# Optimization experiments

Measured on AMD Instinct MI355X. Metric: run time of the kernel, lower is better.

The kernel has to match this reference:

```python
import jax, jax.numpy as jnp
import numpy as np
from jax import lax

EPS = 1e-3  # Keras BatchNormalization default epsilon


def _hard_sigmoid(x):
    # Keras recurrent_activation default for ConvLSTM2D
    return jnp.clip(0.2 * x + 0.5, 0.0, 1.0)


def _conv(x, w, padding):
    # x: [B, Cin, H, W], w: [Cout, Cin, kh, kw]
    return lax.conv_general_dilated(
        x, w, window_strides=(1, 1), padding=padding,
        dimension_numbers=("NCHW", "OIHW", "NCHW"))


def _sympad(x):
    # tf.pad(..., [[0,0],[0,0],[0,0],[1,1],[1,1]], 'SYMMETRIC') on [B,T,C,H,W]
    return jnp.pad(x, ((0, 0), (0, 0), (0, 0), (1, 1), (1, 1)), mode="symmetric")


def _convlstm(xpad, h0, c0, W, U, b):
    # xpad: [B, T, Cin, H+2, W+2]; input conv 'VALID' -> HxW; recurrent conv 'SAME'.
    # Keras gate order along the 4F channel axis: i, f, c(g), o.
    # activation='sigmoid' (candidate/output), recurrent_activation=hard_sigmoid.
    def step(carry, x_t):
        h, c = carry
        z = _conv(x_t, W, "VALID") + _conv(h, U, "SAME") + b[None, :, None, None]
        i, f, g, o = jnp.split(z, 4, axis=1)
        c_new = _hard_sigmoid(f) * c + _hard_sigmoid(i) * jax.nn.sigmoid(g)
        h_new = _hard_sigmoid(o) * jax.nn.sigmoid(c_new)
        return (h_new, c_new), h_new

    (hT, cT), hs = lax.scan(step, (h0, c0), jnp.moveaxis(xpad, 1, 0))
    return jnp.moveaxis(hs, 0, 1), hT, cT  # [B,T,F,H,W], [B,F,H,W] x2


def setup_inputs() -> dict:
    key = jax.random.key(0)
    ks = jax.random.split(key, 5)
    B, T, C, H, Wd, F = 4, 12, 4, 60, 80, 64
    z = lambda: jnp.zeros((B, F, H, Wd), jnp.float32)
    return {
        "inputs": jax.random.normal(ks[0], (B, T, C, H, Wd), jnp.float32),
        "h1_0": z(), "c1_0": z(), "h2_0": z(), "c2_0": z(),
        "W1": jax.random.normal(ks[1], (4 * F, C, 3, 3), jnp.float32) * 0.05,
        "U1": jax.random.normal(ks[2], (4 * F, F, 3, 3), jnp.float32) * 0.05,
        "b1": jnp.zeros((4 * F,), jnp.float32),
        "W2": jax.random.normal(ks[3], (4 * F, F, 3, 3), jnp.float32) * 0.05,
        "U2": jax.random.normal(ks[4], (4 * F, F, 3, 3), jnp.float32) * 0.05,
        "b2": jnp.zeros((4 * F,), jnp.float32),
        "gamma": jnp.ones((Wd,), jnp.float32),
        "beta": jnp.zeros((Wd,), jnp.float32),
    }


def reference(inputs, h1_0, c1_0, h2_0, c2_0, W1, U1, b1, W2, U2, b2, gamma, beta):
    x, h1, c1 = _convlstm(_sympad(inputs), h1_0, c1_0, W1, U1, b1)
    # BatchNorm, Keras default axis=-1 (the W axis here), training-mode batch stats.
    mean = jnp.mean(x, axis=(0, 1, 2, 3), keepdims=True)
    var = jnp.var(x, axis=(0, 1, 2, 3), keepdims=True)
    x = (x - mean) * lax.rsqrt(var + EPS) * gamma + beta
    x, h2, c2 = _convlstm(_sympad(x), h2_0, c2_0, W2, U2, b2)
    # dropout treated as identity (deterministic reference)
    return (x, h1, c1, h2, c2)
```

## Files before the change

kernel.cpp:

```cpp
#include <hip/hip_runtime.h>
#include <hip/hip_bf16.h>

typedef __hip_bfloat16 bf16;
typedef __attribute__((ext_vector_type(8))) short sh8;
typedef __attribute__((ext_vector_type(4))) short sh4;
typedef __attribute__((ext_vector_type(4))) float f32x4;

#define HWp 4800
#define Wd 80
#define Hd 60
#define Fh 64
#define Bn 4
#define Tn 12
#define KYS 5248
#define sHT ((long)Fh*HWp)

__device__ __forceinline__ float b2f(bf16 v){ return __bfloat162float(v); }
__device__ __forceinline__ bf16 f2b(float v){ return __float2bfloat16(v); }
__device__ __forceinline__ float bits2f(short s){
    return __uint_as_float(((unsigned)(unsigned short)s) << 16);
}
__device__ __forceinline__ short f2bits(float f){
    bf16 t = f2b(f); short s; __builtin_memcpy(&s, &t, 2); return s;
}

__global__ void perm_w_kernel(const float* __restrict__ src, float* __restrict__ dst, int cin){
    int idx = blockIdx.x*256 + threadIdx.x;
    int n = 256*cin*9;
    if (idx >= n) return;
    int co = idx/(cin*9); int r = idx - co*(cin*9);
    int g = co >> 6, fo = co & 63;
    dst[(fo*4+g)*cin*9 + r] = src[idx];
}
__global__ void perm_bias_kernel(const float* __restrict__ src, float* __restrict__ dst){
    int idx = threadIdx.x;
    int g = idx >> 6, fo = idx & 63;
    dst[fo*4+g] = src[idx];
}
__global__ void pack_w_kernel(const float* __restrict__ U, short* __restrict__ Apk){
    int d = blockIdx.x*256 + threadIdx.x;
    if (d >= 147456) return;
    int j = d & 7, l = (d>>3) & 63, ct = (d>>9) & 15, oc = d >> 13;
    int o = oc >> 1, cc = oc & 1;
    int co = ct*16 + (l & 15);
    int ci = cc*32 + (l>>4)*8 + j;
    Apk[d] = f2bits(U[(co*Fh + ci)*9 + o]);
}

__global__ void copy_f32_kernel(const float* __restrict__ src, float* __restrict__ dst, int n){
    int idx = blockIdx.x*256+threadIdx.x;
    if (idx < n) dst[idx] = src[idx];
}
__global__ void copy_h_f32_kernel(const float* __restrict__ src, long bstride, float* __restrict__ dst){
    long idx = (long)blockIdx.x*256+threadIdx.x;
    long n = (long)Bn*Fh*HWp;
    if (idx >= n) return;
    long b = idx/(Fh*HWp); long r = idx - b*(Fh*HWp);
    dst[idx] = src[b*bstride + r];
}
__global__ void h0cl_kernel(const float* __restrict__ src, bf16* __restrict__ dst){
    long idx = (long)blockIdx.x*256 + threadIdx.x;
    if (idx >= (long)Bn*Fh*HWp) return;
    int fo = (int)(idx & 63);
    long rest = idx >> 6;
    int p = (int)(rest % HWp);
    int b = (int)(rest / HWp);
    dst[idx] = f2b(src[((long)b*Fh + fo)*HWp + p]);
}

__global__ void zx1_kernel(const float* __restrict__ xin,
                           const float* __restrict__ Wf,
                           const float* __restrict__ bias,
                           short* __restrict__ zx)
{
    int p = blockIdx.x*blockDim.x + threadIdx.x;
    if (p >= HWp) return;
    int fo = blockIdx.y, bt = blockIdx.z;
    int y = p / Wd, x = p - y*Wd;
    const float* wf = Wf + fo*4*4*9;
    float acc[4] = {bias[fo*4+0], bias[fo*4+1], bias[fo*4+2], bias[fo*4+3]};
    int ym = (y > 0 ? y-1 : 0)*Wd, y0 = y*Wd, yp = (y < Hd-1 ? y+1 : Hd-1)*Wd;
    int xm = (x > 0 ? x-1 : 0),    xp = (x < Wd-1 ? x+1 : Wd-1);
    for (int ci = 0; ci < 4; ++ci){
        const float* ic = xin + ((long)bt*4 + ci)*HWp;
        float v[9];
        v[0]=ic[ym+xm]; v[1]=ic[ym+x]; v[2]=ic[ym+xp];
        v[3]=ic[y0+xm]; v[4]=ic[y0+x]; v[5]=ic[y0+xp];
        v[6]=ic[yp+xm]; v[7]=ic[yp+x]; v[8]=ic[yp+xp];
        #pragma unroll
        for (int g = 0; g < 4; ++g){
            const float* w = wf + (g*4+ci)*9;
            acc[g] += v[0]*w[0]+v[1]*w[1]+v[2]*w[2]
                    + v[3]*w[3]+v[4]*w[4]+v[5]*w[5]
                    + v[6]*w[6]+v[7]*w[7]+v[8]*w[8];
        }
    }
    sh4 o4 = { f2bits(acc[0]), f2bits(acc[1]), f2bits(acc[2]), f2bits(acc[3]) };
    *(sh4*)(zx + ((long)bt*HWp + p)*256 + fo*4) = o4;
}

template<bool CLAMP>
__device__ __forceinline__ void stage_cl(const short* __restrict__ src, int y, short* lt){
    const int tid = threadIdx.x;
    #pragma unroll
    for (int it = 0; it < 8; ++it){
        int n = it*256 + tid;
        if (n < 1968){
            int row = n/656, rem = n - row*656;
            int rg = y + row - 1;
            bool rvalid = CLAMP ? true : (rg >= 0 && rg < Hd);
            rg = min(max(rg,0), Hd-1);
            int xg, cc, xl; bool cvalid = true;
            if (rem < 640){ xg = rem>>3; cc = rem&7; xl = xg+1; }
            else if (rem < 648){ xg = 0; cc = rem-640; xl = 0; cvalid = CLAMP; }
            else { xg = Wd-1; cc = rem-648; xl = 81; cvalid = CLAMP; }
            sh8 v = {0,0,0,0,0,0,0,0};
            if (rvalid && cvalid) v = *(const sh8*)(src + ((long)(rg*Wd + xg)*64 + cc*8));
            *(sh8*)(lt + row*KYS + xl*64 + ((cc ^ (xl&7))<<3)) = v;
        }
    }
}

__device__ __forceinline__ void gemm_core(const short* __restrict__ Apk, const short* lt,
                                          int wv, int lane, f32x4 acc[4][5]){
    const int lane15 = lane & 15, grp = lane >> 4;
    #pragma unroll
    for (int o = 0; o < 9; ++o){
        int ky = o/3, kx = o - 3*(o/3);
        const short* lk = lt + ky*KYS;
        #pragma unroll
        for (int c = 0; c < 2; ++c){
            sh8 bfr[5];
            #pragma unroll
            for (int pt = 0; pt < 5; ++pt){
                int xl = pt*16 + lane15 + kx;
                int cc = (c*4 + grp) ^ (xl & 7);
                bfr[pt] = *(const sh8*)(lk + xl*64 + cc*8);
            }
            const short* ab = Apk + ((long)((o*2 + c)*16 + wv))*512 + lane*8;
            #pragma unroll
            for (int g = 0; g < 4; ++g){
                sh8 af = *(const sh8*)(ab + (long)g*4*512);
                #pragma unroll
                for (int pt = 0; pt < 5; ++pt)
                    acc[g][pt] = __builtin_amdgcn_mfma_f32_16x16x32_bf16(af, bfr[pt], acc[g][pt], 0, 0, 0);
            }
        }
    }
}

template<bool WRITE_FX>
__global__ __launch_bounds__(256) void rec_step(
    const bf16* __restrict__ hprev, long h_bstride,
    const short* __restrict__ Upk,
    const short* __restrict__ zx_t, long z_bstride,
    float* __restrict__ c,
    bf16* __restrict__ hout,
    float* __restrict__ fx, long f_bstride)
{
    __shared__ short lt[3*KYS];
    int y = blockIdx.x, b = blockIdx.y;
    int tid = threadIdx.x, lane = tid & 63, wv = tid >> 6;
    int lane15 = lane & 15, grp = lane >> 4;

    stage_cl<false>((const short*)hprev + (long)b*h_bstride, y, lt);

    sh4 zq[5][4]; float cold[5][4];
    const short* zb = zx_t + (long)b*z_bstride;
    #pragma unroll
    for (int pt = 0; pt < 5; ++pt){
        int p = y*Wd + pt*16 + lane15;
        #pragma unroll
        for (int r = 0; r < 4; ++r){
            int fo = wv*16 + grp*4 + r;
            zq[pt][r] = *(const sh4*)(zb + (long)p*256 + fo*4);
            cold[pt][r] = c[((long)b*Fh + fo)*HWp + p];
        }
    }
    __syncthreads();

    f32x4 acc[4][5];
    #pragma unroll
    for (int g = 0; g < 4; ++g)
        #pragma unroll
        for (int pt = 0; pt < 5; ++pt) acc[g][pt] = (f32x4){0.f,0.f,0.f,0.f};
    gemm_core(Upk, lt, wv, lane, acc);

    #pragma unroll
    for (int pt = 0; pt < 5; ++pt){
        int p = y*Wd + pt*16 + lane15;
        #pragma unroll
        for (int r = 0; r < 4; ++r){
            int fo = wv*16 + grp*4 + r;
            float zi = acc[0][pt][r] + bits2f(zq[pt][r][0]);
            float zf = acc[1][pt][r] + bits2f(zq[pt][r][1]);
            float zg = acc[2][pt][r] + bits2f(zq[pt][r][2]);
            float zo = acc[3][pt][r] + bits2f(zq[pt][r][3]);
            float gi = fminf(fmaxf(0.2f*zi+0.5f, 0.f), 1.f);
            float gf = fminf(fmaxf(0.2f*zf+0.5f, 0.f), 1.f);
            float go = fminf(fmaxf(0.2f*zo+0.5f, 0.f), 1.f);
            float sg = 1.f/(1.f+__expf(-zg));
            float cn = gf*cold[pt][r] + gi*sg;
            float hn = go * (1.f/(1.f+__expf(-cn)));
            c[((long)b*Fh + fo)*HWp + p] = cn;
            hout[((long)b*sHT) + (long)p*64 + fo] = f2b(hn);
            if (WRITE_FX)
                fx[(long)b*f_bstride + (long)fo*HWp + p] = hn;
        }
    }
}

__global__ __launch_bounds__(256,2) void zx_mfma(
    const bf16* __restrict__ x1,
    const short* __restrict__ Wpk,
    const float* __restrict__ bias,
    short* __restrict__ zxb)
{
    __shared__ short lt[3*KYS];
    int y = blockIdx.x, img = blockIdx.y;
    int t = img / Bn, b = img - t*Bn;
    int tid = threadIdx.x, lane = tid & 63, wv = tid >> 6;
    int lane15 = lane & 15, grp = lane >> 4;
    stage_cl<true>((const short*)x1 + (long)img*sHT, y, lt);
    __syncthreads();
    f32x4 acc[4][5];
    #pragma unroll
    for (int g = 0; g < 4; ++g)
        #pragma unroll
        for (int pt = 0; pt < 5; ++pt) acc[g][pt] = (f32x4){0.f,0.f,0.f,0.f};
    gemm_core(Wpk, lt, wv, lane, acc);
    short* zb = zxb + ((long)(b*Tn + t))*HWp*256;
    #pragma unroll
    for (int pt = 0; pt < 5; ++pt){
        int p = y*Wd + pt*16 + lane15;
        #pragma unroll
        for (int r = 0; r < 4; ++r){
            int fo = wv*16 + grp*4 + r;
            sh4 o4 = { f2bits(acc[0][pt][r] + bias[fo]),
                       f2bits(acc[1][pt][r] + bias[64+fo]),
                       f2bits(acc[2][pt][r] + bias[128+fo]),
                       f2bits(acc[3][pt][r] + bias[192+fo]) };
            *(sh4*)(zb + (long)p*256 + fo*4) = o4;
        }
    }
}

#define BN_GRID 480
__global__ void bn_sum_cl(const short* __restrict__ x, float* __restrict__ sums){
    __shared__ float ls[160];
    int tid = threadIdx.x;
    if (tid < 160) ls[tid] = 0.f;
    __syncthreads();
    long gid = (long)blockIdx.x*256 + tid;
    const long nchunk = (long)Bn*Tn*HWp*8;
    float s = 0.f, q = 0.f;
    for (long ch = gid; ch < nchunk; ch += (long)BN_GRID*256){
        sh8 v = *(const sh8*)(x + ch*8);
        #pragma unroll
        for (int j = 0; j < 8; ++j){ float f = bits2f(v[j]); s += f; q += f*f; }
    }
    int w = (int)((gid>>3) % Wd);
    atomicAdd(&ls[w], s); atomicAdd(&ls[80+w], q);
    __syncthreads();
    if (tid < 160) atomicAdd(&sums[tid], ls[tid]);
}
__global__ void bn_coef_kernel(const float* __restrict__ sums, const float* __restrict__ g,
                               const float* __restrict__ bt, float* __restrict__ coef){
    int w = threadIdx.x;
    const float N = (float)(Bn*Tn*Fh*Hd);
    float mean = sums[w]/N;
    float var  = sums[80+w]/N - mean*mean;
    float sc = rsqrtf(var + 1e-3f)*g[w];
    coef[w] = sc;
    coef[80+w] = bt[w] - mean*sc;
}
__global__ void bn_apply_cl(short* __restrict__ x, const float* __restrict__ coef){
    long gid = (long)blockIdx.x*256 + threadIdx.x;
    const long nchunk = (long)Bn*Tn*HWp*8;
    int w = (int)((gid>>3) % Wd);
    float sc = coef[w], sh = coef[80+w];
    for (long ch = gid; ch < nchunk; ch += (long)BN_GRID*256){
        sh8 v = *(sh8*)(x + ch*8);
        #pragma unroll
        for (int j = 0; j < 8; ++j) v[j] = f2bits(bits2f(v[j])*sc + sh);
        *(sh8*)(x + ch*8) = v;
    }
}

extern "C" void kernel_launch(void* const* d_in, const int* in_sizes, int n_in,
                              void* d_out, int out_size, void* d_ws, size_t ws_size,
                              hipStream_t stream){
    const float* xin  = (const float*)d_in[0];
    const float* h1_0 = (const float*)d_in[1];
    const float* c1_0 = (const float*)d_in[2];
    const float* h2_0 = (const float*)d_in[3];
    const float* c2_0 = (const float*)d_in[4];
    const float* W1   = (const float*)d_in[5];
    const float* U1   = (const float*)d_in[6];
    const float* b1   = (const float*)d_in[7];
    const float* W2   = (const float*)d_in[8];
    const float* U2   = (const float*)d_in[9];
    const float* b2   = (const float*)d_in[10];
    const float* gamma= (const float*)d_in[11];
    const float* beta = (const float*)d_in[12];
    float* out = (float*)d_out;

    char* ws = (char*)d_ws;
    float* W1f = (float*)ws; ws += (size_t)256*4*9*4;
    float* b1f = (float*)ws; ws += 1024;
    short* U1p = (short*)ws; ws += (size_t)147456*2;
    short* W2p = (short*)ws; ws += (size_t)147456*2;
    short* U2p = (short*)ws; ws += (size_t)147456*2;
    float* sums= (float*)ws; ws += 1024;
    float* coef= (float*)ws; ws += 1024;
    float* cbuf= (float*)ws; ws += (size_t)Bn*Fh*HWp*4;
    bf16*  h0b = (bf16*)ws; ws += (size_t)Bn*Fh*HWp*2;
    bf16*  hdb = (bf16*)ws; ws += (size_t)2*Bn*Fh*HWp*2;
    bf16*  x1  = (bf16*)ws; ws += (size_t)Bn*Tn*Fh*HWp*2;
    short* zx  = (short*)ws; ws += (size_t)Bn*Tn*256*HWp*2;

    const long nImg = (long)Bn*Fh*HWp;
    const long xOff = (long)Bn*Tn*Fh*HWp;
    int nImgB = (int)((nImg+255)/256);

    perm_w_kernel<<<(256*4*9+255)/256, 256, 0, stream>>>(W1, W1f, 4);
    perm_bias_kernel<<<1,256,0,stream>>>(b1, b1f);
    pack_w_kernel<<<576,256,0,stream>>>(U1, U1p);
    pack_w_kernel<<<576,256,0,stream>>>(W2, W2p);
    pack_w_kernel<<<576,256,0,stream>>>(U2, U2p);

    dim3 rgrid(Hd, Bn);
    const long zstep = (long)HWp*256;
    const long zbstr = (long)Tn*HWp*256;

    dim3 zgrid1((HWp+255)/256, 64, Bn*Tn);
    zx1_kernel<<<zgrid1,256,0,stream>>>(xin, W1f, b1f, zx);
    copy_f32_kernel<<<nImgB,256,0,stream>>>(c1_0, cbuf, (int)nImg);
    h0cl_kernel<<<nImgB,256,0,stream>>>(h1_0, h0b);
    for (int t = 0; t < Tn; ++t){
        const bf16* hp = (t==0) ? h0b : x1 + (long)(t-1)*Bn*sHT;
        bf16* ho = x1 + (long)t*Bn*sHT;
        if (t == Tn-1)
            rec_step<true><<<rgrid,256,0,stream>>>(hp, sHT, U1p,
                zx + (long)t*zstep, zbstr, cbuf, ho, out + xOff, sHT);
        else
            rec_step<false><<<rgrid,256,0,stream>>>(hp, sHT, U1p,
                zx + (long)t*zstep, zbstr, cbuf, ho, nullptr, 0);
    }
    copy_f32_kernel<<<nImgB,256,0,stream>>>(cbuf, out + xOff + nImg, (int)nImg);

    hipMemsetAsync(sums, 0, 640, stream);
    bn_sum_cl<<<BN_GRID,256,0,stream>>>((const short*)x1, sums);
    bn_coef_kernel<<<1,80,0,stream>>>(sums, gamma, beta, coef);
    bn_apply_cl<<<BN_GRID,256,0,stream>>>((short*)x1, coef);

    dim3 zgrid2(Hd, Bn*Tn);
    zx_mfma<<<zgrid2,256,0,stream>>>(x1, W2p, b2, zx);
    copy_f32_kernel<<<nImgB,256,0,stream>>>(c2_0, cbuf, (int)nImg);
    h0cl_kernel<<<nImgB,256,0,stream>>>(h2_0, h0b);
    for (int t = 0; t < Tn; ++t){
        const bf16* hp = (t==0) ? h0b : hdb + (long)((t-1)&1)*Bn*sHT;
        bf16* ho = hdb + (long)(t&1)*Bn*sHT;
        rec_step<true><<<rgrid,256,0,stream>>>(hp, sHT, U2p,
            zx + (long)t*zstep, zbstr, cbuf, ho, out + (long)t*sHT, (long)Tn*sHT);
    }
    copy_h_f32_kernel<<<nImgB,256,0,stream>>>(out + (long)(Tn-1)*sHT, (long)Tn*sHT, out + xOff + 2*nImg);
    copy_f32_kernel<<<nImgB,256,0,stream>>>(cbuf, out + xOff + 3*nImg, (int)nImg);
}
```

Before: 998.4 us.

## Split recurrent step over feature halves and change zx layout to channel-major

The recurrent step kernel now launches twice as many blocks of 128 threads, each handling half of the 64 output feature tiles, so the 240-block grid becomes 480 blocks for better CU occupancy on the serial time loop. The zx gate buffer is stored feature-major (fo, pixel, gate) instead of pixel-major, making the per-lane loads contiguous across pixels. h outputs are staged through shared memory for coalesced channel-last writes. The cost is staging the 3-row halo of h twice (once per half) and an extra barrier.

New measurement: 1.004 ms. About the same (+0.6%).

```diff
diff --git a/kernel.cpp b/kernel.cpp
--- a/kernel.cpp
+++ b/kernel.cpp
@@ -14,6 +14,7 @@
 #define Tn 12
 #define KYS 5248
 #define sHT ((long)Fh*HWp)
+#define ZT  ((long)Fh*HWp*4)
 
 __device__ __forceinline__ float b2f(bf16 v){ return __bfloat162float(v); }
 __device__ __forceinline__ bf16 f2b(float v){ return __float2bfloat16(v); }
@@ -96,28 +97,24 @@
         }
     }
     sh4 o4 = { f2bits(acc[0]), f2bits(acc[1]), f2bits(acc[2]), f2bits(acc[3]) };
-    *(sh4*)(zx + ((long)bt*HWp + p)*256 + fo*4) = o4;
-}
-
-template<bool CLAMP>
+    *(sh4*)(zx + (((long)bt*Fh + fo)*HWp + p)*4) = o4;
+}
+
+template<bool CLAMP, int NT>
 __device__ __forceinline__ void stage_cl(const short* __restrict__ src, int y, short* lt){
     const int tid = threadIdx.x;
-    #pragma unroll
-    for (int it = 0; it < 8; ++it){
-        int n = it*256 + tid;
-        if (n < 1968){
-            int row = n/656, rem = n - row*656;
-            int rg = y + row - 1;
-            bool rvalid = CLAMP ? true : (rg >= 0 && rg < Hd);
-            rg = min(max(rg,0), Hd-1);
-            int xg, cc, xl; bool cvalid = true;
-            if (rem < 640){ xg = rem>>3; cc = rem&7; xl = xg+1; }
-            else if (rem < 648){ xg = 0; cc = rem-640; xl = 0; cvalid = CLAMP; }
-            else { xg = Wd-1; cc = rem-648; xl = 81; cvalid = CLAMP; }
-            sh8 v = {0,0,0,0,0,0,0,0};
-            if (rvalid && cvalid) v = *(const sh8*)(src + ((long)(rg*Wd + xg)*64 + cc*8));
-            *(sh8*)(lt + row*KYS + xl*64 + ((cc ^ (xl&7))<<3)) = v;
-        }
+    for (int n = tid; n < 1968; n += NT){
+        int row = n/656, rem = n - row*656;
+        int rg = y + row - 1;
+        bool rvalid = CLAMP ? true : (rg >= 0 && rg < Hd);
+        rg = min(max(rg,0), Hd-1);
+        int xg, cc, xl; bool cvalid = true;
+        if (rem < 640){ xg = rem>>3; cc = rem&7; xl = xg+1; }
+        else if (rem < 648){ xg = 0; cc = rem-640; xl = 0; cvalid = CLAMP; }
+        else { xg = Wd-1; cc = rem-648; xl = 81; cvalid = CLAMP; }
+        sh8 v = {0,0,0,0,0,0,0,0};
+        if (rvalid && cvalid) v = *(const sh8*)(src + ((long)(rg*Wd + xg)*64 + cc*8));
+        *(sh8*)(lt + row*KYS + xl*64 + ((cc ^ (xl&7))<<3)) = v;
     }
 }
 
@@ -150,7 +147,7 @@
 }
 
 template<bool WRITE_FX>
-__global__ __launch_bounds__(256) void rec_step(
+__global__ __launch_bounds__(128) void rec_step(
     const bf16* __restrict__ hprev, long h_bstride,
     const short* __restrict__ Upk,
     const short* __restrict__ zx_t, long z_bstride,
@@ -159,11 +156,13 @@
     float* __restrict__ fx, long f_bstride)
 {
     __shared__ short lt[3*KYS];
-    int y = blockIdx.x, b = blockIdx.y;
+    __shared__ short lo[80*36];
+    int y = blockIdx.x, b = blockIdx.y, fh = blockIdx.z;
     int tid = threadIdx.x, lane = tid & 63, wv = tid >> 6;
     int lane15 = lane & 15, grp = lane >> 4;
-
-    stage_cl<false>((const short*)hprev + (long)b*h_bstride, y, lt);
+    int ft = fh*2 + wv;
+
+    stage_cl<false,128>((const short*)hprev + (long)b*h_bstride, y, lt);
 
     sh4 zq[5][4]; float cold[5][4];
     const short* zb = zx_t + (long)b*z_bstride;
@@ -172,8 +171,8 @@
         int p = y*Wd + pt*16 + lane15;
         #pragma unroll
         for (int r = 0; r < 4; ++r){
-            int fo = wv*16 + grp*4 + r;
-            zq[pt][r] = *(const sh4*)(zb + (long)p*256 + fo*4);
+            int fo = ft*16 + grp*4 + r;
+            zq[pt][r] = *(const sh4*)(zb + ((long)fo*HWp + p)*4);
             cold[pt][r] = c[((long)b*Fh + fo)*HWp + p];
         }
     }
@@ -184,14 +183,38 @@
     for (int g = 0; g < 4; ++g)
         #pragma unroll
         for (int pt = 0; pt < 5; ++pt) acc[g][pt] = (f32x4){0.f,0.f,0.f,0.f};
-    gemm_core(Upk, lt, wv, lane, acc);
+
+    #pragma unroll
+    for (int o = 0; o < 9; ++o){
+        int ky = o/3, kx = o - 3*(o/3);
+        const short* lk = lt + ky*KYS;
+        #pragma unroll
+        for (int cch = 0; cch < 2; ++cch){
+            sh8 bfr[5];
+            #pragma unroll
+            for (int pt = 0; pt < 5; ++pt){
+                int xl = pt*16 + lane15 + kx;
+                int cc = (cch*4 + grp) ^ (xl & 7);
+                bfr[pt] = *(const sh8*)(lk + xl*64 + cc*8);
+            }
+            const short* ab = Upk + ((long)((o*2 + cch)*16 + ft))*512 + lane*8;
+            #pragma unroll
+            for (int g = 0; g < 4; ++g){
+                sh8 af = *(const sh8*)(ab + (long)g*4*512);
+                #pragma unroll
+                for (int pt = 0; pt < 5; ++pt)
+                    acc[g][pt] = __builtin_amdgcn_mfma_f32_16x16x32_bf16(af, bfr[pt], acc[g][pt], 0, 0, 0);
+            }
+        }
+    }
 
     #pragma unroll
     for (int pt = 0; pt < 5; ++pt){
-        int p = y*Wd + pt*16 + lane15;
+        int pl = pt*16 + lane15;
+        int p = y*Wd + pl;
         #pragma unroll
         for (int r = 0; r < 4; ++r){
-            int fo = wv*16 + grp*4 + r;
+            int fo = ft*16 + grp*4 + r;
             float zi = acc[0][pt][r] + bits2f(zq[pt][r][0]);
             float zf = acc[1][pt][r] + bits2f(zq[pt][r][1]);
             float zg = acc[2][pt][r] + bits2f(zq[pt][r][2]);
@@ -203,10 +226,19 @@
             float cn = gf*cold[pt][r] + gi*sg;
             float hn = go * (1.f/(1.f+__expf(-cn)));
             c[((long)b*Fh + fo)*HWp + p] = cn;
-            hout[((long)b*sHT) + (long)p*64 + fo] = f2b(hn);
+            lo[pl*36 + wv*16 + grp*4 + r] = f2bits(hn);
             if (WRITE_FX)
                 fx[(long)b*f_bstride + (long)fo*HWp + p] = hn;
         }
+    }
+    __syncthreads();
+    short* hb = (short*)hout + (long)b*sHT;
+    #pragma unroll
+    for (int k = 0; k < 5; ++k){
+        int e = k*128 + tid;
+        int pl = e >> 3, f4 = (e & 7)*4;
+        sh4 hv = *(const sh4*)(lo + pl*36 + f4);
+        *(sh4*)(hb + (long)(y*Wd + pl)*64 + fh*32 + f4) = hv;
     }
 }
 
@@ -221,7 +253,7 @@
     int t = img / Bn, b = img - t*Bn;
     int tid = threadIdx.x, lane = tid & 63, wv = tid >> 6;
     int lane15 = lane & 15, grp = lane >> 4;
-    stage_cl<true>((const short*)x1 + (long)img*sHT, y, lt);
+    stage_cl<true,256>((const short*)x1 + (long)img*sHT, y, lt);
     __syncthreads();
     f32x4 acc[4][5];
     #pragma unroll
@@ -229,7 +261,7 @@
         #pragma unroll
         for (int pt = 0; pt < 5; ++pt) acc[g][pt] = (f32x4){0.f,0.f,0.f,0.f};
     gemm_core(Wpk, lt, wv, lane, acc);
-    short* zb = zxb + ((long)(b*Tn + t))*HWp*256;
+    short* zb = zxb + ((long)(b*Tn + t))*ZT;
     #pragma unroll
     for (int pt = 0; pt < 5; ++pt){
         int p = y*Wd + pt*16 + lane15;
@@ -240,7 +272,7 @@
                        f2bits(acc[1][pt][r] + bias[64+fo]),
                        f2bits(acc[2][pt][r] + bias[128+fo]),
                        f2bits(acc[3][pt][r] + bias[192+fo]) };
-            *(sh4*)(zb + (long)p*256 + fo*4) = o4;
+            *(sh4*)(zb + ((long)fo*HWp + p)*4) = o4;
         }
     }
 }
@@ -329,9 +361,8 @@
     pack_w_kernel<<<576,256,0,stream>>>(W2, W2p);
     pack_w_kernel<<<576,256,0,stream>>>(U2, U2p);
 
-    dim3 rgrid(Hd, Bn);
-    const long zstep = (long)HWp*256;
-    const long zbstr = (long)Tn*HWp*256;
+    dim3 rgrid(Hd, Bn, 2);
+    const long zbstr = (long)Tn*ZT;
 
     dim3 zgrid1((HWp+255)/256, 64, Bn*Tn);
     zx1_kernel<<<zgrid1,256,0,stream>>>(xin, W1f, b1f, zx);
@@ -341,11 +372,11 @@
         const bf16* hp = (t==0) ? h0b : x1 + (long)(t-1)*Bn*sHT;
         bf16* ho = x1 + (long)t*Bn*sHT;
         if (t == Tn-1)
-            rec_step<true><<<rgrid,256,0,stream>>>(hp, sHT, U1p,
-                zx + (long)t*zstep, zbstr, cbuf, ho, out + xOff, sHT);
+            rec_step<true><<<rgrid,128,0,stream>>>(hp, sHT, U1p,
+                zx + (long)t*ZT, zbstr, cbuf, ho, out + xOff, sHT);
         else
-            rec_step<false><<<rgrid,256,0,stream>>>(hp, sHT, U1p,
-                zx + (long)t*zstep, zbstr, cbuf, ho, nullptr, 0);
+            rec_step<false><<<rgrid,128,0,stream>>>(hp, sHT, U1p,
+                zx + (long)t*ZT, zbstr, cbuf, ho, nullptr, 0);
     }
     copy_f32_kernel<<<nImgB,256,0,stream>>>(cbuf, out + xOff + nImg, (int)nImg);
 
@@ -361,8 +392,8 @@
     for (int t = 0; t < Tn; ++t){
         const bf16* hp = (t==0) ? h0b : hdb + (long)((t-1)&1)*Bn*sHT;
         bf16* ho = hdb + (long)(t&1)*Bn*sHT;
-        rec_step<true><<<rgrid,256,0,stream>>>(hp, sHT, U2p,
-            zx + (long)t*zstep, zbstr, cbuf, ho, out + (long)t*sHT, (long)Tn*sHT);
+        rec_step<true><<<rgrid,128,0,stream>>>(hp, sHT, U2p,
+            zx + (long)t*ZT, zbstr, cbuf, ho, out + (long)t*sHT, (long)Tn*sHT);
     }
     copy_h_f32_kernel<<<nImgB,256,0,stream>>>(out + (long)(Tn-1)*sHT, (long)Tn*sHT, out + xOff + 2*nImg);
     copy_f32_kernel<<<nImgB,256,0,stream>>>(cbuf, out + xOff + 3*nImg, (int)nImg);
```
